# Kernel optimization log

Measured on AMD Instinct MI355X. Metric: run time of the kernel, lower is better.

Reference implementation:

```python
import jax, jax.numpy as jnp
import numpy as np

B, T, C = 2, 2048, 1024
NH = 16
HD = C // NH
SCALE = 1.0 / np.sqrt(HD).astype(np.float32)


def setup_inputs() -> dict:
    key = jax.random.key(0)
    k1, k2, k3 = jax.random.split(key, 3)
    x = jax.random.normal(k1, (B, T, C), dtype=jnp.float32)
    # torch Linear stores weight (out,in) and computes x @ W^T; we store the
    # transposed (in,out) layout directly, scaled like default init.
    w_qkv = jax.random.normal(k2, (C, 3 * C), dtype=jnp.float32) * (1.0 / np.sqrt(C))
    w_proj = jax.random.normal(k3, (C, C), dtype=jnp.float32) * (1.0 / np.sqrt(C))
    return {"x": x, "w_qkv": w_qkv, "w_proj": w_proj}


def reference(x, w_qkv, w_proj):
    b, t, c = x.shape
    qkv = x @ w_qkv                                  # (b, t, 3c)
    q, k, v = jnp.split(qkv, 3, axis=-1)
    q = q.reshape(b, t, NH, HD)
    k = k.reshape(b, t, NH, HD)
    v = v.reshape(b, t, NH, HD)
    # scores: (b, nh, t, t) — full materialization, faithful to the original
    att = jnp.einsum("bthd,bshd->bhts", q, k) * SCALE
    causal = jnp.tril(jnp.ones((t, t), dtype=bool))  # (t, t)
    neg = jnp.finfo(att.dtype).min
    att = jnp.where(causal[None, None, :, :], att, neg)
    weights = jax.nn.softmax(att, axis=-1)
    y = jnp.einsum("bhts,bshd->bthd", weights, v).reshape(b, t, c)
    y = y @ w_proj
    return y
```

## Files before the change

kernel.cpp:

```cpp
#include <hip/hip_runtime.h>
#include <hip/hip_bf16.h>
#include <stdint.h>

typedef __bf16 bf16x8 __attribute__((ext_vector_type(8)));
typedef float f32x4 __attribute__((ext_vector_type(4)));
typedef unsigned short us4v __attribute__((ext_vector_type(4)));
typedef unsigned short us8v __attribute__((ext_vector_type(8)));

#define B_   2
#define T_   2048
#define C_   1024
#define NH_  16
#define HD_  64

__device__ __forceinline__ unsigned short f2bf(float f) {
  unsigned int u = __builtin_bit_cast(unsigned int, f);
  u += 0x7fffu + ((u >> 16) & 1u);
  return (unsigned short)(u >> 16);
}
__device__ __forceinline__ float bf2f(unsigned short u) {
  unsigned int x = ((unsigned int)u) << 16;
  return __builtin_bit_cast(float, x);
}

__device__ __forceinline__ void gload16(const void* g, void* l) {
  __builtin_amdgcn_global_load_lds(
      (const __attribute__((address_space(1))) unsigned int*)g,
      (__attribute__((address_space(3))) unsigned int*)l, 16, 0, 0);
}

__device__ __forceinline__ f32x4 mfma16(bf16x8 a, bf16x8 b, f32x4 c) {
  return __builtin_amdgcn_mfma_f32_16x16x32_bf16(a, b, c, 0, 0, 0);
}

__global__ __launch_bounds__(256) void cast_x_kernel(const float4* __restrict__ in,
                                                     us4v* __restrict__ out) {
  int i = blockIdx.x * 256 + threadIdx.x;
  float4 f = in[i];
  us4v o; o[0] = f2bf(f.x); o[1] = f2bf(f.y); o[2] = f2bf(f.z); o[3] = f2bf(f.w);
  out[i] = o;
}

__global__ __launch_bounds__(256) void transpose_cast_kernel(const float* __restrict__ w,
                                                             unsigned short* __restrict__ wT,
                                                             int K, int N) {
  __shared__ float tile[32][33];
  int n0 = blockIdx.x * 32, k0 = blockIdx.y * 32;
  int tx = threadIdx.x, ty = threadIdx.y;
  #pragma unroll
  for (int i = 0; i < 4; ++i)
    tile[ty + 8*i][tx] = w[(size_t)(k0 + ty + 8*i) * N + n0 + tx];
  __syncthreads();
  #pragma unroll
  for (int i = 0; i < 4; ++i)
    wT[(size_t)(n0 + ty + 8*i) * K + k0 + tx] = f2bf(tile[tx][ty + 8*i]);
}

__device__ __forceinline__ void gemm_core(const unsigned short* __restrict__ A,
                                          const unsigned short* __restrict__ Bt,
                                          int K, int m0, int n0,
                                          unsigned short* lA, unsigned short* lB,
                                          f32x4 acc[4][4]) {
  const int t = threadIdx.x;
  const int lane = t & 63, w = t >> 6;
  const int wm = w >> 1, wn = w & 1;
  const int g = lane >> 4, r16 = lane & 15;
  #pragma unroll
  for (int i = 0; i < 4; ++i)
    #pragma unroll
    for (int j = 0; j < 4; ++j) acc[i][j] = (f32x4){0.f, 0.f, 0.f, 0.f};

  for (int k0 = 0; k0 < K; k0 += 64) {
    #pragma unroll
    for (int i = 0; i < 4; ++i) {
      int slot = i * 256 + t;
      int r = slot >> 3, p = slot & 7;
      int q = p ^ (r & 7);
      gload16(A  + (size_t)(m0 + r) * K + k0 + q * 8, lA + slot * 8);
      gload16(Bt + (size_t)(n0 + r) * K + k0 + q * 8, lB + slot * 8);
    }
    asm volatile("s_waitcnt vmcnt(0)" ::: "memory");
    __syncthreads();

    bf16x8 af[4][2], bfr[4][2];
    #pragma unroll
    for (int mi = 0; mi < 4; ++mi)
      #pragma unroll
      for (int kk = 0; kk < 2; ++kk) {
        int r = wm * 64 + mi * 16 + r16;
        int ps = (kk * 4 + g) ^ (r & 7);
        af[mi][kk] = *(const bf16x8*)(lA + r * 64 + ps * 8);
      }
    #pragma unroll
    for (int ni = 0; ni < 4; ++ni)
      #pragma unroll
      for (int kk = 0; kk < 2; ++kk) {
        int r = wn * 64 + ni * 16 + r16;
        int ps = (kk * 4 + g) ^ (r & 7);
        bfr[ni][kk] = *(const bf16x8*)(lB + r * 64 + ps * 8);
      }
    #pragma unroll
    for (int mi = 0; mi < 4; ++mi)
      #pragma unroll
      for (int ni = 0; ni < 4; ++ni)
        #pragma unroll
        for (int kk = 0; kk < 2; ++kk)
          acc[mi][ni] = mfma16(af[mi][kk], bfr[ni][kk], acc[mi][ni]);
    __syncthreads();
  }
}

__device__ __forceinline__ int xcd_swz(int flat, int nwg) {
  int cpx = nwg >> 3;
  return (flat & 7) * cpx + (flat >> 3);
}

__global__ __launch_bounds__(256) void gemm_qkv_kernel(const unsigned short* __restrict__ xb,
                                                       const unsigned short* __restrict__ wT,
                                                       unsigned short* __restrict__ qb,
                                                       unsigned short* __restrict__ kb,
                                                       unsigned short* __restrict__ vb) {
  __shared__ unsigned short lA[128 * 64];
  __shared__ unsigned short lB[128 * 64];
  f32x4 acc[4][4];
  const int nbx = 3 * C_ / 128;
  int flat = xcd_swz(blockIdx.y * nbx + blockIdx.x, nbx * ((B_ * T_) / 128));
  const int m0 = (flat / nbx) * 128, n0 = (flat % nbx) * 128;
  gemm_core(xb, wT, C_, m0, n0, lA, lB, acc);
  const int t = threadIdx.x, lane = t & 63, w = t >> 6;
  const int wm = w >> 1, wn = w & 1, g = lane >> 4, r16 = lane & 15;
  #pragma unroll
  for (int mi = 0; mi < 4; ++mi)
    #pragma unroll
    for (int ni = 0; ni < 4; ++ni)
      #pragma unroll
      for (int j = 0; j < 4; ++j) {
        int gm = m0 + wm * 64 + mi * 16 + g * 4 + j;
        int gn = n0 + wn * 64 + ni * 16 + r16;
        int b = gm >> 11, tt = gm & 2047;
        int s = gn >> 10, rem = gn & 1023;
        int h = rem >> 6, d = rem & 63;
        unsigned short val = f2bf(acc[mi][ni][j]);
        size_t idx = ((size_t)(b * NH_ + h) * T_ + tt) * HD_ + d;
        if (s == 0)      qb[idx] = val;
        else if (s == 1) kb[idx] = val;
        else             vb[idx] = val;
      }
}

__global__ __launch_bounds__(256) void gemm_proj_kernel(const unsigned short* __restrict__ ab,
                                                        const unsigned short* __restrict__ wT,
                                                        float* __restrict__ out) {
  __shared__ unsigned short lA[128 * 64];
  __shared__ unsigned short lB[128 * 64];
  f32x4 acc[4][4];
  const int nbx = C_ / 128;
  int flat = xcd_swz(blockIdx.y * nbx + blockIdx.x, nbx * ((B_ * T_) / 128));
  const int m0 = (flat / nbx) * 128, n0 = (flat % nbx) * 128;
  gemm_core(ab, wT, C_, m0, n0, lA, lB, acc);
  const int t = threadIdx.x, lane = t & 63, w = t >> 6;
  const int wm = w >> 1, wn = w & 1, g = lane >> 4, r16 = lane & 15;
  #pragma unroll
  for (int mi = 0; mi < 4; ++mi)
    #pragma unroll
    for (int ni = 0; ni < 4; ++ni)
      #pragma unroll
      for (int j = 0; j < 4; ++j) {
        int gm = m0 + wm * 64 + mi * 16 + g * 4 + j;
        int gn = n0 + wn * 64 + ni * 16 + r16;
        out[(size_t)gm * C_ + gn] = acc[mi][ni][j];
      }
}

__global__ __launch_bounds__(256, 4) void attn_kernel(const unsigned short* __restrict__ qb,
                                                      const unsigned short* __restrict__ kb,
                                                      const unsigned short* __restrict__ vb,
                                                      unsigned short* __restrict__ ao,
                                                      unsigned short* __restrict__ partB,
                                                      float* __restrict__ mlbuf) {
  __shared__ unsigned short LDS[20480];
  const int L = blockIdx.x;
  const int inner = L >> 3;
  const int bh = (L & 7) * 4 + (inner / 24);
  const int pidx = inner % 24;
  const int pseg = pidx >> 3, pp = pidx & 7;
  int t0, kvLo, kvHi, mode;
  if (pseg == 0)      { t0 = 16 + 2 * pp;          kvLo = 0;  kvHi = 16;          mode = 1; }
  else if (pseg == 1) { int q = 7 - pp; t0 = 2 * q;      kvLo = 0;  kvHi = 2 * q + 2;  mode = 0; }
  else                { int q = 7 - pp; t0 = 16 + 2 * q; kvLo = 16; kvHi = 18 + 2 * q; mode = 2; }
  const int len = kvHi - kvLo;
  const int t = threadIdx.x, lane = t & 63, w4 = t >> 6;
  const int g = lane >> 4, r16 = lane & 15;
  const int tsel = w4 >> 1, hsel = w4 & 1;
  const int myTile = t0 + tsel;
  const int qt0w = myTile * 64 + hsel * 32;
  const int myLim = min(len, myTile + 1 - kvLo);

  const unsigned short* Q  = qb + (size_t)bh * (T_ * HD_);
  const unsigned short* Kp = kb + (size_t)bh * (T_ * HD_);
  const unsigned short* Vp = vb + (size_t)bh * (T_ * HD_);

  bf16x8 qf[2][2];
  #pragma unroll
  for (int h = 0; h < 2; ++h) {
    int qrow = qt0w + h * 16 + r16;
    #pragma unroll
    for (int kk = 0; kk < 2; ++kk) {
      us8v raw = *(const us8v*)(Q + (size_t)qrow * HD_ + kk * 32 + g * 8);
      bf16x8 qv;
      #pragma unroll
      for (int j = 0; j < 8; ++j) qv[j] = (__bf16)(bf2f(raw[j]) * 0.125f);
      qf[h][kk] = qv;
    }
  }

  f32x4 o[2][4];
  #pragma unroll
  for (int h = 0; h < 2; ++h)
    #pragma unroll
    for (int c = 0; c < 4; ++c) o[h][c] = (f32x4){0.f, 0.f, 0.f, 0.f};
  float mrun[2] = {-__builtin_inff(), -__builtin_inff()};
  float lrun[2] = {0.f, 0.f};

  const int kr0 = t >> 3,         kp0 = (t & 7) ^ (kr0 & 7);
  const int kr1 = (t + 256) >> 3, kp1 = (t & 7) ^ (kr1 & 7);
  const int colp = (lane & 32) | ((lane & 12) << 1) | ((lane >> 2) & 4) | (lane & 3);
  const int cslot = colp >> 3, cwithin = colp & 7;

  gload16(Kp + (size_t)(kvLo * 64 + kr0) * HD_ + kp0 * 8, LDS + t * 8);
  gload16(Kp + (size_t)(kvLo * 64 + kr1) * HD_ + kp1 * 8, LDS + (t + 256) * 8);
  us8v nvA0 = *(const us8v*)(Vp + (size_t)(kvLo * 64 + lane) * HD_ + w4 * 16);
  us8v nvA1 = *(const us8v*)(Vp + (size_t)(kvLo * 64 + lane) * HD_ + w4 * 16 + 8);
  us8v nvB0, nvB1;
  if (len > 1) {
    const int k1 = (kvLo + 1) * 64;
    gload16(Kp + (size_t)(k1 + kr0) * HD_ + kp0 * 8, LDS + 4096 + t * 8);
    gload16(Kp + (size_t)(k1 + kr1) * HD_ + kp1 * 8, LDS + 4096 + (t + 256) * 8);
    nvB0 = *(const us8v*)(Vp + (size_t)(k1 + lane) * HD_ + w4 * 16);
    nvB1 = *(const us8v*)(Vp + (size_t)(k1 + lane) * HD_ + w4 * 16 + 8);
  }

  for (int ii = 0; ii < len; ++ii) {
    const int it = kvLo + ii;
    const unsigned short* Kl = LDS + (ii % 3) * 4096;
    unsigned short* Vt = LDS + 12288 + (ii & 1) * 4096;

    if (ii + 1 < len) { asm volatile("s_waitcnt vmcnt(4)" ::: "memory"); }
    else              { asm volatile("s_waitcnt vmcnt(0)" ::: "memory"); }
    {
      us8v v0, v1;
      if (ii & 1) { v0 = nvB0; v1 = nvB1; } else { v0 = nvA0; v1 = nvA1; }
      #pragma unroll
      for (int u = 0; u < 8; ++u) {
        int d = w4 * 16 + u;
        Vt[d * 64 + ((cslot ^ u) << 3) + cwithin] = v0[u];
      }
      #pragma unroll
      for (int u = 0; u < 8; ++u) {
        int d = w4 * 16 + 8 + u;
        Vt[d * 64 + ((cslot ^ u) << 3) + cwithin] = v1[u];
      }
    }
    __syncthreads();

    if (ii + 2 < len) {
      const int kn = (it + 2) * 64;
      unsigned short* Kn = LDS + ((ii + 2) % 3) * 4096;
      gload16(Kp + (size_t)(kn + kr0) * HD_ + kp0 * 8, Kn + t * 8);
      gload16(Kp + (size_t)(kn + kr1) * HD_ + kp1 * 8, Kn + (t + 256) * 8);
      if (ii & 1) {
        nvB0 = *(const us8v*)(Vp + (size_t)(kn + lane) * HD_ + w4 * 16);
        nvB1 = *(const us8v*)(Vp + (size_t)(kn + lane) * HD_ + w4 * 16 + 8);
      } else {
        nvA0 = *(const us8v*)(Vp + (size_t)(kn + lane) * HD_ + w4 * 16);
        nvA1 = *(const us8v*)(Vp + (size_t)(kn + lane) * HD_ + w4 * 16 + 8);
      }
    }

    if (ii < myLim) {
      f32x4 s4t[2][4];
      #pragma unroll
      for (int h = 0; h < 2; ++h)
        #pragma unroll
        for (int c = 0; c < 4; ++c) s4t[h][c] = (f32x4){0.f, 0.f, 0.f, 0.f};
      __builtin_amdgcn_s_setprio(1);
      #pragma unroll
      for (int c = 0; c < 4; ++c)
        #pragma unroll
        for (int kk = 0; kk < 2; ++kk) {
          int r = c * 16 + r16;
          int ps = (kk * 4 + g) ^ (r & 7);
          bf16x8 kf = *(const bf16x8*)(Kl + r * 64 + ps * 8);
          s4t[0][c] = mfma16(kf, qf[0][kk], s4t[0][c]);
          s4t[1][c] = mfma16(kf, qf[1][kk], s4t[1][c]);
        }
      __builtin_amdgcn_s_setprio(0);
      if (it == myTile) {
        #pragma unroll
        for (int h = 0; h < 2; ++h) {
          int qloc = hsel * 32 + h * 16 + r16;
          #pragma unroll
          for (int c = 0; c < 4; ++c)
            #pragma unroll
            for (int j = 0; j < 4; ++j)
              if (c * 16 + g * 4 + j > qloc) s4t[h][c][j] = -1e30f;
        }
      }
      bf16x8 pf[2][2];
      #pragma unroll
      for (int h = 0; h < 2; ++h) {
        float mx = -1e30f;
        #pragma unroll
        for (int c = 0; c < 4; ++c)
          #pragma unroll
          for (int j = 0; j < 4; ++j) mx = fmaxf(mx, s4t[h][c][j]);
        mx = fmaxf(mx, __shfl_xor(mx, 16));
        mx = fmaxf(mx, __shfl_xor(mx, 32));
        float mn = fmaxf(mrun[h], mx);
        float alpha = __expf(mrun[h] - mn);
        mrun[h] = mn;
        float rs = 0.f;
        #pragma unroll
        for (int c = 0; c < 4; ++c)
          #pragma unroll
          for (int j = 0; j < 4; ++j) {
            float p = __expf(s4t[h][c][j] - mn);
            s4t[h][c][j] = p;
            rs += p;
          }
        rs += __shfl_xor(rs, 16);
        rs += __shfl_xor(rs, 32);
        lrun[h] = lrun[h] * alpha + rs;
        #pragma unroll
        for (int c = 0; c < 4; ++c)
          #pragma unroll
          for (int j = 0; j < 4; ++j) o[h][c][j] *= alpha;
        #pragma unroll
        for (int kk = 0; kk < 2; ++kk) {
          bf16x8 p;
          #pragma unroll
          for (int j = 0; j < 4; ++j) {
            p[j]     = (__bf16)s4t[h][2 * kk][j];
            p[4 + j] = (__bf16)s4t[h][2 * kk + 1][j];
          }
          pf[h][kk] = p;
        }
      }
      __builtin_amdgcn_s_setprio(1);
      #pragma unroll
      for (int c = 0; c < 4; ++c) {
        int rv = c * 16 + r16;
        #pragma unroll
        for (int kk = 0; kk < 2; ++kk) {
          int slot = (4 * kk + g) ^ (r16 & 7);
          bf16x8 vf = *(const bf16x8*)(Vt + rv * 64 + slot * 8);
          o[0][c] = mfma16(vf, pf[0][kk], o[0][c]);
          o[1][c] = mfma16(vf, pf[1][kk], o[1][c]);
        }
      }
      __builtin_amdgcn_s_setprio(0);
    }
  }

  unsigned short* ep = LDS + (len % 3) * 4096 + w4 * 1024;
  #pragma unroll
  for (int h = 0; h < 2; ++h) {
    if (mode && g == 0) {
      int prow = (bh * 16 + (myTile - 16)) * 64 + hsel * 32 + h * 16 + r16;
      float* mlp = mlbuf + (size_t)prow * 4;
      if (mode == 1) { mlp[0] = mrun[h]; mlp[1] = lrun[h]; }
      else           { mlp[2] = mrun[h]; mlp[3] = lrun[h]; }
    }
    float inv = 1.f / lrun[h];
    #pragma unroll
    for (int c = 0; c < 4; ++c) {
      us4v pk;
      #pragma unroll
      for (int j = 0; j < 4; ++j) pk[j] = f2bf(o[h][c][j] * inv);
      int slot = (4 * c + g) ^ r16;
      *(us4v*)(ep + r16 * 64 + slot * 4) = pk;
    }
    asm volatile("s_waitcnt lgkmcnt(0)" ::: "memory");
    __builtin_amdgcn_sched_barrier(0);
    {
      int q = lane >> 2, seg = lane & 3;
      us4v a0 = *(const us4v*)(ep + q * 64 + (((seg * 4 + 0) ^ q) & 15) * 4);
      us4v a1 = *(const us4v*)(ep + q * 64 + (((seg * 4 + 1) ^ q) & 15) * 4);
      us4v a2 = *(const us4v*)(ep + q * 64 + (((seg * 4 + 2) ^ q) & 15) * 4);
      us4v a3 = *(const us4v*)(ep + q * 64 + (((seg * 4 + 3) ^ q) & 15) * 4);
      us8v o0 = {a0[0],a0[1],a0[2],a0[3],a1[0],a1[1],a1[2],a1[3]};
      us8v o1 = {a2[0],a2[1],a2[2],a2[3],a3[0],a3[1],a3[2],a3[3]};
      if (mode != 2) {
        size_t rowg = (size_t)(bh >> 4) * T_ + qt0w + h * 16 + q;
        int colg = (bh & 15) * 64 + seg * 16;
        *(us8v*)(ao + rowg * C_ + colg)     = o0;
        *(us8v*)(ao + rowg * C_ + colg + 8) = o1;
      } else {
        size_t prow = (size_t)(bh * 16 + (myTile - 16)) * 64 + hsel * 32 + h * 16 + q;
        *(us8v*)(partB + prow * 64 + seg * 16)     = o0;
        *(us8v*)(partB + prow * 64 + seg * 16 + 8) = o1;
      }
    }
    asm volatile("s_waitcnt lgkmcnt(0)" ::: "memory");
    __builtin_amdgcn_sched_barrier(0);
  }
}

__global__ __launch_bounds__(256) void attn_merge_kernel(unsigned short* __restrict__ ao,
                                                         const unsigned short* __restrict__ partB,
                                                         const float* __restrict__ mlbuf) {
  const int blk = blockIdx.x;
  const int bh = blk >> 4, ti = blk & 15;
  const int t = threadIdx.x;
  const int row = t >> 2, seg = t & 3;
  const size_t prow = (size_t)(bh * 16 + ti) * 64 + row;
  const float* mlp = mlbuf + prow * 4;
  float mA = mlp[0], lA = mlp[1], mB = mlp[2], lB = mlp[3];
  float m = fmaxf(mA, mB);
  float wA = lA * __expf(mA - m), wB = lB * __expf(mB - m);
  float rinv = 1.f / (wA + wB);
  wA *= rinv; wB *= rinv;
  size_t rowg = (size_t)(bh >> 4) * T_ + (16 + ti) * 64 + row;
  unsigned short* aop = ao + rowg * C_ + (bh & 15) * 64 + seg * 16;
  const unsigned short* obp = partB + prow * 64 + seg * 16;
  us8v oa0 = *(const us8v*)(aop);
  us8v oa1 = *(const us8v*)(aop + 8);
  us8v ob0 = *(const us8v*)(obp);
  us8v ob1 = *(const us8v*)(obp + 8);
  us8v r0, r1;
  #pragma unroll
  for (int j = 0; j < 8; ++j) {
    r0[j] = f2bf(bf2f(oa0[j]) * wA + bf2f(ob0[j]) * wB);
    r1[j] = f2bf(bf2f(oa1[j]) * wA + bf2f(ob1[j]) * wB);
  }
  *(us8v*)(aop)     = r0;
  *(us8v*)(aop + 8) = r1;
}

extern "C" void kernel_launch(void* const* d_in, const int* in_sizes, int n_in,
                              void* d_out, int out_size, void* d_ws, size_t ws_size,
                              hipStream_t stream) {
  const float* x      = (const float*)d_in[0];
  const float* w_qkv  = (const float*)d_in[1];
  const float* w_proj = (const float*)d_in[2];
  float* out = (float*)d_out;
  char* ws = (char*)d_ws;

  unsigned short* xb     = (unsigned short*)(ws);
  unsigned short* wqkvT  = (unsigned short*)(ws + 8388608);
  unsigned short* wprojT = (unsigned short*)(ws + 14680064);
  unsigned short* qb     = (unsigned short*)(ws + 16777216);
  unsigned short* kb     = (unsigned short*)(ws + 25165824);
  unsigned short* vb     = (unsigned short*)(ws + 33554432);
  unsigned short* ao     = xb;
  unsigned short* partB  = wqkvT;
  float*          mlbuf  = (float*)(ws + 8388608 + 4194304);

  cast_x_kernel<<<4096, 256, 0, stream>>>((const float4*)x, (us4v*)xb);
  transpose_cast_kernel<<<dim3(3 * C_ / 32, C_ / 32), dim3(32, 8), 0, stream>>>(
      w_qkv, wqkvT, C_, 3 * C_);
  transpose_cast_kernel<<<dim3(C_ / 32, C_ / 32), dim3(32, 8), 0, stream>>>(
      w_proj, wprojT, C_, C_);
  gemm_qkv_kernel<<<dim3(3 * C_ / 128, (B_ * T_) / 128), 256, 0, stream>>>(
      xb, wqkvT, qb, kb, vb);
  attn_kernel<<<dim3(768), 256, 0, stream>>>(qb, kb, vb, ao, partB, mlbuf);
  attn_merge_kernel<<<512, 256, 0, stream>>>(ao, partB, mlbuf);
  gemm_proj_kernel<<<dim3(C_ / 128, (B_ * T_) / 128), 256, 0, stream>>>(
      ao, wprojT, out);
}
```

Baseline: 141.4 us.

## Merge prep kernels, split attention into single-tile blocks, add lazy softmax rescale

Folds the x cast and both weight transpose-casts into one prep kernel launch, removing two launches. Restructures the attention kernel so each 128-thread block handles a single 64-row query tile instead of two tiles per 256-thread block, doubling the grid and dropping per-warp iteration limits. Softmax now skips the running-max rescale of the accumulator unless the new max exceeds the old by more than 8, cutting exp and multiply work but allowing exponentials up to e^8 relative to the stored max.

Result: faster. 137.3 us (-2.9%).

```diff
diff --git a/kernel.cpp b/kernel.cpp
--- a/kernel.cpp
+++ b/kernel.cpp
@@ -33,27 +33,34 @@
   return __builtin_amdgcn_mfma_f32_16x16x32_bf16(a, b, c, 0, 0, 0);
 }
 
-__global__ __launch_bounds__(256) void cast_x_kernel(const float4* __restrict__ in,
-                                                     us4v* __restrict__ out) {
-  int i = blockIdx.x * 256 + threadIdx.x;
-  float4 f = in[i];
-  us4v o; o[0] = f2bf(f.x); o[1] = f2bf(f.y); o[2] = f2bf(f.z); o[3] = f2bf(f.w);
-  out[i] = o;
-}
-
-__global__ __launch_bounds__(256) void transpose_cast_kernel(const float* __restrict__ w,
-                                                             unsigned short* __restrict__ wT,
-                                                             int K, int N) {
+__global__ __launch_bounds__(256) void prep_kernel(const float* __restrict__ x,
+                                                   unsigned short* __restrict__ xb,
+                                                   const float* __restrict__ w_qkv,
+                                                   unsigned short* __restrict__ wqkvT,
+                                                   const float* __restrict__ w_proj,
+                                                   unsigned short* __restrict__ wprojT) {
   __shared__ float tile[32][33];
-  int n0 = blockIdx.x * 32, k0 = blockIdx.y * 32;
-  int tx = threadIdx.x, ty = threadIdx.y;
+  const int b = blockIdx.x, t = threadIdx.x;
+  if (b < 4096) {
+    int i = b * 256 + t;
+    float4 f = ((const float4*)x)[i];
+    us4v o; o[0] = f2bf(f.x); o[1] = f2bf(f.y); o[2] = f2bf(f.z); o[3] = f2bf(f.w);
+    ((us4v*)xb)[i] = o;
+    return;
+  }
+  const float* w; unsigned short* wT; int N, tb;
+  if (b < 7168) { tb = b - 4096; w = w_qkv;  wT = wqkvT;  N = 3 * C_; }
+  else          { tb = b - 7168; w = w_proj; wT = wprojT; N = C_; }
+  const int nx = N / 32;
+  const int n0 = (tb % nx) * 32, k0 = (tb / nx) * 32;
+  const int tx = t & 31, ty = t >> 5;
   #pragma unroll
   for (int i = 0; i < 4; ++i)
     tile[ty + 8*i][tx] = w[(size_t)(k0 + ty + 8*i) * N + n0 + tx];
   __syncthreads();
   #pragma unroll
   for (int i = 0; i < 4; ++i)
-    wT[(size_t)(n0 + ty + 8*i) * K + k0 + tx] = f2bf(tile[tx][ty + 8*i]);
+    wT[(size_t)(n0 + ty + 8*i) * C_ + k0 + tx] = f2bf(tile[tx][ty + 8*i]);
 }
 
 __device__ __forceinline__ void gemm_core(const unsigned short* __restrict__ A,
@@ -172,7 +179,7 @@
       }
 }
 
-__global__ __launch_bounds__(256, 4) void attn_kernel(const unsigned short* __restrict__ qb,
+__global__ __launch_bounds__(128, 2) void attn_kernel(const unsigned short* __restrict__ qb,
                                                       const unsigned short* __restrict__ kb,
                                                       const unsigned short* __restrict__ vb,
                                                       unsigned short* __restrict__ ao,
@@ -181,20 +188,16 @@
   __shared__ unsigned short LDS[20480];
   const int L = blockIdx.x;
   const int inner = L >> 3;
-  const int bh = (L & 7) * 4 + (inner / 24);
-  const int pidx = inner % 24;
-  const int pseg = pidx >> 3, pp = pidx & 7;
-  int t0, kvLo, kvHi, mode;
-  if (pseg == 0)      { t0 = 16 + 2 * pp;          kvLo = 0;  kvHi = 16;          mode = 1; }
-  else if (pseg == 1) { int q = 7 - pp; t0 = 2 * q;      kvLo = 0;  kvHi = 2 * q + 2;  mode = 0; }
-  else                { int q = 7 - pp; t0 = 16 + 2 * q; kvLo = 16; kvHi = 18 + 2 * q; mode = 2; }
+  const int bh = (L & 7) * 4 + (inner / 48);
+  const int bx = inner % 48;
+  int tile, kvLo, kvHi, mode;
+  if (bx < 16)      { tile = 16 + bx; kvLo = 0;  kvHi = 16;       mode = 1; }
+  else if (bx < 32) { tile = 47 - bx; kvLo = 16; kvHi = tile + 1; mode = 2; }
+  else              { tile = 47 - bx; kvLo = 0;  kvHi = tile + 1; mode = 0; }
+  const int qt0 = tile * 64;
   const int len = kvHi - kvLo;
-  const int t = threadIdx.x, lane = t & 63, w4 = t >> 6;
+  const int t = threadIdx.x, lane = t & 63, w2 = t >> 6;
   const int g = lane >> 4, r16 = lane & 15;
-  const int tsel = w4 >> 1, hsel = w4 & 1;
-  const int myTile = t0 + tsel;
-  const int qt0w = myTile * 64 + hsel * 32;
-  const int myLim = min(len, myTile + 1 - kvLo);
 
   const unsigned short* Q  = qb + (size_t)bh * (T_ * HD_);
   const unsigned short* Kp = kb + (size_t)bh * (T_ * HD_);
@@ -203,7 +206,7 @@
   bf16x8 qf[2][2];
   #pragma unroll
   for (int h = 0; h < 2; ++h) {
-    int qrow = qt0w + h * 16 + r16;
+    int qrow = qt0 + w2 * 32 + h * 16 + r16;
     #pragma unroll
     for (int kk = 0; kk < 2; ++kk) {
       us8v raw = *(const us8v*)(Q + (size_t)qrow * HD_ + kk * 32 + g * 8);
@@ -222,22 +225,34 @@
   float mrun[2] = {-__builtin_inff(), -__builtin_inff()};
   float lrun[2] = {0.f, 0.f};
 
-  const int kr0 = t >> 3,         kp0 = (t & 7) ^ (kr0 & 7);
-  const int kr1 = (t + 256) >> 3, kp1 = (t & 7) ^ (kr1 & 7);
+  const int kr0 = (t +   0) >> 3, kp0 = (t & 7) ^ (kr0 & 7);
+  const int kr1 = (t + 128) >> 3, kp1 = (t & 7) ^ (kr1 & 7);
+  const int kr2 = (t + 256) >> 3, kp2 = (t & 7) ^ (kr2 & 7);
+  const int kr3 = (t + 384) >> 3, kp3 = (t & 7) ^ (kr3 & 7);
   const int colp = (lane & 32) | ((lane & 12) << 1) | ((lane >> 2) & 4) | (lane & 3);
   const int cslot = colp >> 3, cwithin = colp & 7;
-
-  gload16(Kp + (size_t)(kvLo * 64 + kr0) * HD_ + kp0 * 8, LDS + t * 8);
-  gload16(Kp + (size_t)(kvLo * 64 + kr1) * HD_ + kp1 * 8, LDS + (t + 256) * 8);
-  us8v nvA0 = *(const us8v*)(Vp + (size_t)(kvLo * 64 + lane) * HD_ + w4 * 16);
-  us8v nvA1 = *(const us8v*)(Vp + (size_t)(kvLo * 64 + lane) * HD_ + w4 * 16 + 8);
-  us8v nvB0, nvB1;
+  const int dbase = w2 * 32;
+
+#define AK_STAGE(kv0, buf)                                                     \
+  {                                                                            \
+    unsigned short* Kd = LDS + (buf) * 4096;                                   \
+    gload16(Kp + (size_t)((kv0) + kr0) * HD_ + kp0 * 8, Kd + (t +   0) * 8);   \
+    gload16(Kp + (size_t)((kv0) + kr1) * HD_ + kp1 * 8, Kd + (t + 128) * 8);   \
+    gload16(Kp + (size_t)((kv0) + kr2) * HD_ + kp2 * 8, Kd + (t + 256) * 8);   \
+    gload16(Kp + (size_t)((kv0) + kr3) * HD_ + kp3 * 8, Kd + (t + 384) * 8);   \
+  }
+#define AV_LOAD(kv0, n0, n1, n2, n3)                                           \
+  n0 = *(const us8v*)(Vp + (size_t)((kv0) + lane) * HD_ + dbase +  0);         \
+  n1 = *(const us8v*)(Vp + (size_t)((kv0) + lane) * HD_ + dbase +  8);         \
+  n2 = *(const us8v*)(Vp + (size_t)((kv0) + lane) * HD_ + dbase + 16);         \
+  n3 = *(const us8v*)(Vp + (size_t)((kv0) + lane) * HD_ + dbase + 24);
+
+  us8v nvA0, nvA1, nvA2, nvA3, nvB0, nvB1, nvB2, nvB3;
+  AK_STAGE(kvLo * 64, 0);
+  AV_LOAD(kvLo * 64, nvA0, nvA1, nvA2, nvA3);
   if (len > 1) {
-    const int k1 = (kvLo + 1) * 64;
-    gload16(Kp + (size_t)(k1 + kr0) * HD_ + kp0 * 8, LDS + 4096 + t * 8);
-    gload16(Kp + (size_t)(k1 + kr1) * HD_ + kp1 * 8, LDS + 4096 + (t + 256) * 8);
-    nvB0 = *(const us8v*)(Vp + (size_t)(k1 + lane) * HD_ + w4 * 16);
-    nvB1 = *(const us8v*)(Vp + (size_t)(k1 + lane) * HD_ + w4 * 16 + 8);
+    AK_STAGE((kvLo + 1) * 64, 1);
+    AV_LOAD((kvLo + 1) * 64, nvB0, nvB1, nvB2, nvB3);
   }
 
   for (int ii = 0; ii < len; ++ii) {
@@ -245,39 +260,43 @@
     const unsigned short* Kl = LDS + (ii % 3) * 4096;
     unsigned short* Vt = LDS + 12288 + (ii & 1) * 4096;
 
-    if (ii + 1 < len) { asm volatile("s_waitcnt vmcnt(4)" ::: "memory"); }
+    if (ii + 1 < len) { asm volatile("s_waitcnt vmcnt(8)" ::: "memory"); }
     else              { asm volatile("s_waitcnt vmcnt(0)" ::: "memory"); }
     {
-      us8v v0, v1;
-      if (ii & 1) { v0 = nvB0; v1 = nvB1; } else { v0 = nvA0; v1 = nvA1; }
+      us8v v0, v1, v2, v3;
+      if (ii & 1) { v0 = nvB0; v1 = nvB1; v2 = nvB2; v3 = nvB3; }
+      else        { v0 = nvA0; v1 = nvA1; v2 = nvA2; v3 = nvA3; }
       #pragma unroll
       for (int u = 0; u < 8; ++u) {
-        int d = w4 * 16 + u;
+        int d = dbase + u;
         Vt[d * 64 + ((cslot ^ u) << 3) + cwithin] = v0[u];
       }
       #pragma unroll
       for (int u = 0; u < 8; ++u) {
-        int d = w4 * 16 + 8 + u;
+        int d = dbase + 8 + u;
         Vt[d * 64 + ((cslot ^ u) << 3) + cwithin] = v1[u];
+      }
+      #pragma unroll
+      for (int u = 0; u < 8; ++u) {
+        int d = dbase + 16 + u;
+        Vt[d * 64 + ((cslot ^ u) << 3) + cwithin] = v2[u];
+      }
+      #pragma unroll
+      for (int u = 0; u < 8; ++u) {
+        int d = dbase + 24 + u;
+        Vt[d * 64 + ((cslot ^ u) << 3) + cwithin] = v3[u];
       }
     }
     __syncthreads();
 
     if (ii + 2 < len) {
       const int kn = (it + 2) * 64;
-      unsigned short* Kn = LDS + ((ii + 2) % 3) * 4096;
-      gload16(Kp + (size_t)(kn + kr0) * HD_ + kp0 * 8, Kn + t * 8);
-      gload16(Kp + (size_t)(kn + kr1) * HD_ + kp1 * 8, Kn + (t + 256) * 8);
-      if (ii & 1) {
-        nvB0 = *(const us8v*)(Vp + (size_t)(kn + lane) * HD_ + w4 * 16);
-        nvB1 = *(const us8v*)(Vp + (size_t)(kn + lane) * HD_ + w4 * 16 + 8);
-      } else {
-        nvA0 = *(const us8v*)(Vp + (size_t)(kn + lane) * HD_ + w4 * 16);
-        nvA1 = *(const us8v*)(Vp + (size_t)(kn + lane) * HD_ + w4 * 16 + 8);
-      }
-    }
-
-    if (ii < myLim) {
+      AK_STAGE(kn, (ii + 2) % 3);
+      if (ii & 1) { AV_LOAD(kn, nvB0, nvB1, nvB2, nvB3); }
+      else        { AV_LOAD(kn, nvA0, nvA1, nvA2, nvA3); }
+    }
+
+    {
       f32x4 s4t[2][4];
       #pragma unroll
       for (int h = 0; h < 2; ++h)
@@ -295,10 +314,10 @@
           s4t[1][c] = mfma16(kf, qf[1][kk], s4t[1][c]);
         }
       __builtin_amdgcn_s_setprio(0);
-      if (it == myTile) {
+      if (it == tile) {
         #pragma unroll
         for (int h = 0; h < 2; ++h) {
-          int qloc = hsel * 32 + h * 16 + r16;
+          int qloc = w2 * 32 + h * 16 + r16;
           #pragma unroll
           for (int c = 0; c < 4; ++c)
             #pragma unroll
@@ -309,32 +328,36 @@
       bf16x8 pf[2][2];
       #pragma unroll
       for (int h = 0; h < 2; ++h) {
-        float mx = -1e30f;
-        #pragma unroll
-        for (int c = 0; c < 4; ++c)
-          #pragma unroll
-          for (int j = 0; j < 4; ++j) mx = fmaxf(mx, s4t[h][c][j]);
+        float t0 = fmaxf(fmaxf(s4t[h][0][0], s4t[h][0][1]), s4t[h][0][2]);
+        float t1 = fmaxf(fmaxf(s4t[h][0][3], s4t[h][1][0]), s4t[h][1][1]);
+        float t2 = fmaxf(fmaxf(s4t[h][1][2], s4t[h][1][3]), s4t[h][2][0]);
+        float t3 = fmaxf(fmaxf(s4t[h][2][1], s4t[h][2][2]), s4t[h][2][3]);
+        float t4 = fmaxf(fmaxf(s4t[h][3][0], s4t[h][3][1]), s4t[h][3][2]);
+        float mx = fmaxf(fmaxf(fmaxf(t0, t1), fmaxf(t2, t3)),
+                         fmaxf(t4, s4t[h][3][3]));
         mx = fmaxf(mx, __shfl_xor(mx, 16));
         mx = fmaxf(mx, __shfl_xor(mx, 32));
-        float mn = fmaxf(mrun[h], mx);
-        float alpha = __expf(mrun[h] - mn);
-        mrun[h] = mn;
-        float rs = 0.f;
-        #pragma unroll
-        for (int c = 0; c < 4; ++c)
+        if (!__all(mx - mrun[h] <= 8.0f)) {
+          float mn = fmaxf(mrun[h], mx);
+          float alpha = __expf(mrun[h] - mn);
+          mrun[h] = mn;
+          lrun[h] *= alpha;
           #pragma unroll
-          for (int j = 0; j < 4; ++j) {
-            float p = __expf(s4t[h][c][j] - mn);
-            s4t[h][c][j] = p;
-            rs += p;
-          }
+          for (int c = 0; c < 4; ++c)
+            #pragma unroll
+            for (int j = 0; j < 4; ++j) o[h][c][j] *= alpha;
+        }
+        float ps4[4];
+        #pragma unroll
+        for (int c = 0; c < 4; ++c) {
+          #pragma unroll
+          for (int j = 0; j < 4; ++j) s4t[h][c][j] = __expf(s4t[h][c][j] - mrun[h]);
+          ps4[c] = (s4t[h][c][0] + s4t[h][c][1]) + (s4t[h][c][2] + s4t[h][c][3]);
+        }
+        float rs = (ps4[0] + ps4[1]) + (ps4[2] + ps4[3]);
         rs += __shfl_xor(rs, 16);
         rs += __shfl_xor(rs, 32);
-        lrun[h] = lrun[h] * alpha + rs;
-        #pragma unroll
-        for (int c = 0; c < 4; ++c)
-          #pragma unroll
-          for (int j = 0; j < 4; ++j) o[h][c][j] *= alpha;
+        lrun[h] += rs;
         #pragma unroll
         for (int kk = 0; kk < 2; ++kk) {
           bf16x8 p;
@@ -362,11 +385,11 @@
     }
   }
 
-  unsigned short* ep = LDS + (len % 3) * 4096 + w4 * 1024;
+  unsigned short* ep = LDS + (len % 3) * 4096 + w2 * 1024;
   #pragma unroll
   for (int h = 0; h < 2; ++h) {
     if (mode && g == 0) {
-      int prow = (bh * 16 + (myTile - 16)) * 64 + hsel * 32 + h * 16 + r16;
+      int prow = (bh * 16 + (tile - 16)) * 64 + w2 * 32 + h * 16 + r16;
       float* mlp = mlbuf + (size_t)prow * 4;
       if (mode == 1) { mlp[0] = mrun[h]; mlp[1] = lrun[h]; }
       else           { mlp[2] = mrun[h]; mlp[3] = lrun[h]; }
@@ -391,12 +414,12 @@
       us8v o0 = {a0[0],a0[1],a0[2],a0[3],a1[0],a1[1],a1[2],a1[3]};
       us8v o1 = {a2[0],a2[1],a2[2],a2[3],a3[0],a3[1],a3[2],a3[3]};
       if (mode != 2) {
-        size_t rowg = (size_t)(bh >> 4) * T_ + qt0w + h * 16 + q;
+        size_t rowg = (size_t)(bh >> 4) * T_ + qt0 + w2 * 32 + h * 16 + q;
         int colg = (bh & 15) * 64 + seg * 16;
         *(us8v*)(ao + rowg * C_ + colg)     = o0;
         *(us8v*)(ao + rowg * C_ + colg + 8) = o1;
       } else {
-        size_t prow = (size_t)(bh * 16 + (myTile - 16)) * 64 + hsel * 32 + h * 16 + q;
+        size_t prow = (size_t)(bh * 16 + (tile - 16)) * 64 + w2 * 32 + h * 16 + q;
         *(us8v*)(partB + prow * 64 + seg * 16)     = o0;
         *(us8v*)(partB + prow * 64 + seg * 16 + 8) = o1;
       }
@@ -404,6 +427,8 @@
     asm volatile("s_waitcnt lgkmcnt(0)" ::: "memory");
     __builtin_amdgcn_sched_barrier(0);
   }
+#undef AK_STAGE
+#undef AV_LOAD
 }
 
 __global__ __launch_bounds__(256) void attn_merge_kernel(unsigned short* __restrict__ ao,
@@ -456,14 +481,10 @@
   unsigned short* partB  = wqkvT;
   float*          mlbuf  = (float*)(ws + 8388608 + 4194304);
 
-  cast_x_kernel<<<4096, 256, 0, stream>>>((const float4*)x, (us4v*)xb);
-  transpose_cast_kernel<<<dim3(3 * C_ / 32, C_ / 32), dim3(32, 8), 0, stream>>>(
-      w_qkv, wqkvT, C_, 3 * C_);
-  transpose_cast_kernel<<<dim3(C_ / 32, C_ / 32), dim3(32, 8), 0, stream>>>(
-      w_proj, wprojT, C_, C_);
+  prep_kernel<<<8192, 256, 0, stream>>>(x, xb, w_qkv, wqkvT, w_proj, wprojT);
   gemm_qkv_kernel<<<dim3(3 * C_ / 128, (B_ * T_) / 128), 256, 0, stream>>>(
       xb, wqkvT, qb, kb, vb);
-  attn_kernel<<<dim3(768), 256, 0, stream>>>(qb, kb, vb, ao, partB, mlbuf);
+  attn_kernel<<<dim3(1536), 128, 0, stream>>>(qb, kb, vb, ao, partB, mlbuf);
   attn_merge_kernel<<<512, 256, 0, stream>>>(ao, partB, mlbuf);
   gemm_proj_kernel<<<dim3(C_ / 128, (B_ * T_) / 128), 256, 0, stream>>>(
       ao, wprojT, out);
```
